# Kernel tuning notes

Measured on AMD Instinct MI355X. Metric: run time of the kernel, lower is better.

Reference implementation:

```python
import jax, jax.numpy as jnp
import numpy as np
from jax import lax

B, S, I, H = 64, 512, 1024, 1024


def _lstm_dir(x, W_ih, W_hh, b_ih, b_hh):
    # x: [B, S, I] -> hidden states [B, S, H]
    # Precompute input projections for all timesteps in one GEMM.
    xg = jnp.einsum('bsi,gi->bsg', x, W_ih) + b_ih + b_hh  # [B, S, 4H]
    Whh_T = W_hh.T  # [H, 4H]
    h0 = jnp.zeros((x.shape[0], W_hh.shape[1]), dtype=x.dtype)
    c0 = jnp.zeros_like(h0)

    def step(carry, xg_t):
        h, c = carry
        g = xg_t + h @ Whh_T  # [B, 4H]
        i_g, f_g, g_g, o_g = jnp.split(g, 4, axis=-1)  # PyTorch gate order i,f,g,o
        i_g = jax.nn.sigmoid(i_g)
        f_g = jax.nn.sigmoid(f_g)
        g_g = jnp.tanh(g_g)
        o_g = jax.nn.sigmoid(o_g)
        c = f_g * c + i_g * g_g
        h = o_g * jnp.tanh(c)
        return (h, c), h

    _, hs = lax.scan(step, (h0, c0), jnp.swapaxes(xg, 0, 1))  # hs: [S, B, H]
    return jnp.swapaxes(hs, 0, 1)


def setup_inputs() -> dict:
    key = jax.random.key(0)
    ks = jax.random.split(key, 10)
    s = 1.0 / np.sqrt(H)  # PyTorch LSTMCell init scale
    return {
        'forward_x': jax.random.normal(ks[0], (B, S, I), jnp.float32),
        'backward_x': jax.random.normal(ks[1], (B, S, I), jnp.float32),
        'W_ih_f': jax.random.uniform(ks[2], (4 * H, I), jnp.float32, -s, s),
        'W_hh_f': jax.random.uniform(ks[3], (4 * H, H), jnp.float32, -s, s),
        'b_ih_f': jax.random.uniform(ks[4], (4 * H,), jnp.float32, -s, s),
        'b_hh_f': jax.random.uniform(ks[5], (4 * H,), jnp.float32, -s, s),
        'W_ih_b': jax.random.uniform(ks[6], (4 * H, I), jnp.float32, -s, s),
        'W_hh_b': jax.random.uniform(ks[7], (4 * H, H), jnp.float32, -s, s),
        'b_ih_b': jax.random.uniform(ks[8], (4 * H,), jnp.float32, -s, s),
        'b_hh_b': jax.random.uniform(ks[9], (4 * H,), jnp.float32, -s, s),
    }


def reference(forward_x, backward_x, W_ih_f, W_hh_f, b_ih_f, b_hh_f,
              W_ih_b, W_hh_b, b_ih_b, b_hh_b):
    fwd = _lstm_dir(forward_x, W_ih_f, W_hh_f, b_ih_f, b_hh_f)
    # Backward direction consumes backward_x from the last timestep to the
    # first and writes hidden states back at their original positions,
    # i.e. run on the time-reversed sequence and reverse the outputs.
    bwd = _lstm_dir(backward_x[:, ::-1, :], W_ih_b, W_hh_b, b_ih_b, b_hh_b)[:, ::-1, :]
    return fwd, bwd
```

## Files before the change

kernel.cpp:

```cpp
#include <hip/hip_runtime.h>
#include <hip/hip_bf16.h>
#include <cstdint>


typedef __bf16 bf16_t;
typedef bf16_t bf16x8 __attribute__((ext_vector_type(8)));
typedef float  f32x4  __attribute__((ext_vector_type(4)));

#define DEVI __device__ __forceinline__

constexpr int Bb = 64, Ss = 512, Ii = 1024, Hh = 1024;
constexpr size_t WS_FLAGS  = 0;
constexpr size_t WS_HRING  = 4096;
constexpr size_t WS_XBF    = 1ull << 20;
constexpr size_t XBF_BYTES = 2ull * Ss * Bb * Ii * 2;
constexpr size_t WS_NEED_XBF = WS_XBF + XBF_BYTES;
constexpr int LDS_TOTAL = 163840;

DEVI float fast_sig(float x) {
  float z = __expf(-fabsf(x));
  float r = __builtin_amdgcn_rcpf(1.f + z);
  return x >= 0.f ? r : z * r;
}
DEVI float fast_tanh(float x) {
  float z = __expf(-2.f * fabsf(x));
  float r = (1.f - z) * __builtin_amdgcn_rcpf(1.f + z);
  return x >= 0.f ? r : -r;
}
DEVI bf16x8 cvt8(f32x4 a, f32x4 b) {
  bf16x8 r;
  r[0] = (bf16_t)a[0]; r[1] = (bf16_t)a[1]; r[2] = (bf16_t)a[2]; r[3] = (bf16_t)a[3];
  r[4] = (bf16_t)b[0]; r[5] = (bf16_t)b[1]; r[6] = (bf16_t)b[2]; r[7] = (bf16_t)b[3];
  return r;
}
DEVI f32x4 mfma16(bf16x8 a, bf16x8 b, f32x4 c) {
  return __builtin_amdgcn_mfma_f32_16x16x32_bf16(a, b, c, 0, 0, 0);
}

#define GLDS16(g, s)                                                           \
  __builtin_amdgcn_global_load_lds(                                            \
      (const __attribute__((address_space(1))) void*)(const void*)(g),         \
      (__attribute__((address_space(3))) void*)(void*)(s), 16, 0, 0)
#define GLDS16_COH(g, s)                                                       \
  __builtin_amdgcn_global_load_lds(                                            \
      (const __attribute__((address_space(1))) void*)(const void*)(g),         \
      (__attribute__((address_space(3))) void*)(void*)(s), 16, 0, 17)
#define WAIT_LGKM0 asm volatile("s_waitcnt lgkmcnt(0)" ::: "memory")
#define WAIT_VM(n) asm volatile("s_waitcnt vmcnt(" #n ")" ::: "memory")
#define BARRIER_RAW                                                            \
  do { __builtin_amdgcn_s_barrier(); __builtin_amdgcn_sched_barrier(0); } while (0)

__global__ void k_init(int* flags) {
  int i = threadIdx.x;
  if (i < 256) flags[i] = 0;
}

__global__ void k_convx(const float* __restrict__ xf, const float* __restrict__ xb,
                        bf16_t* __restrict__ dst) {
  size_t og = (size_t)blockIdx.x * blockDim.x + threadIdx.x;
  int i8  = (int)(og & 127);
  int b   = (int)((og >> 7) & 63);
  int t   = (int)((og >> 13) & 511);
  int dir = (int)(og >> 22);
  const float* src = (dir ? xb : xf) + (((size_t)b * Ss + t) * Ii + (size_t)i8 * 8);
  f32x4 a = *(const f32x4*)src;
  f32x4 c = *(const f32x4*)(src + 4);
  *(bf16x8*)(dst + og * 8) = cvt8(a, c);
}

template <bool XBF>
__global__ void __launch_bounds__(512, 2)
k_lstm(const float* __restrict__ xf, const float* __restrict__ xb,
       const float* __restrict__ Wih_f, const float* __restrict__ Whh_f,
       const float* __restrict__ bih_f, const float* __restrict__ bhh_f,
       const float* __restrict__ Wih_b, const float* __restrict__ Whh_b,
       const float* __restrict__ bih_b, const float* __restrict__ bhh_b,
       float* __restrict__ out,
       const bf16_t* __restrict__ xbfin, bf16_t* __restrict__ hring,
       int* __restrict__ flags) {
  extern __shared__ char lds[];
  char* PA = lds;
  char* PB = lds + 65536;
  float* part = (float*)(lds + 131072);

  const int tid = threadIdx.x;
  const int bid = blockIdx.x;
  const int dir = bid & 1;
  const int db  = bid >> 1;
  const int n0  = db * 8;
  const int w   = tid >> 6, l = tid & 63;
  const int u   = l >> 4, l15 = l & 15;
  const int m   = w & 1;
  const int kq  = w >> 1;

  const float* Wih = dir ? Wih_b : Wih_f;
  const float* Whh = dir ? Whh_b : Whh_f;
  const float* bih = dir ? bih_b : bih_f;
  const float* bhh = dir ? bhh_b : bhh_f;
  const float* x32 = dir ? xb : xf;
  const bf16_t* xbase = xbfin + (size_t)dir * Ss * Bb * Ii;
  bf16_t* hr = hring + (size_t)dir * 2 * Bb * Hh;
  float* outD = out + (size_t)dir * Bb * Ss * Hh;
  int* myflags = flags + dir * 128;

  bf16x8 wr[2][2][4][2];
#pragma unroll
  for (int mat = 0; mat < 2; ++mat)
#pragma unroll
    for (int p = 0; p < 2; ++p)
#pragma unroll
      for (int ks = 0; ks < 4; ++ks)
#pragma unroll
        for (int nt = 0; nt < 2; ++nt) {
          int c = nt * 16 + l15;
          int j = (c >> 3) * 1024 + n0 + (c & 7);
          int k = p * 512 + kq * 128 + ks * 32 + u * 8;
          const float* sp = (mat ? Whh : Wih) + (size_t)j * 1024 + k;
          wr[mat][p][ks][nt] = cvt8(*(const f32x4*)sp, *(const f32x4*)(sp + 4));
        }

  const int eb = tid >> 3, en = tid & 7;
  const int nj = n0 + en;
  float bi0 = bih[nj] + bhh[nj];
  float bi1 = bih[1024 + nj] + bhh[1024 + nj];
  float bi2 = bih[2048 + nj] + bhh[2048 + nj];
  float bi3 = bih[3072 + nj] + bhh[3072 + nj];

  int aoff0[4], aoff1[4];
#pragma unroll
  for (int ks = 0; ks < 4; ++ks) {
    int r0 = m * 32 + l15;
    int r1 = r0 + 16;
    int sl = kq * 16 + ks * 4 + u;
    aoff0[ks] = r0 * 1024 + ((sl ^ (r0 & 7)) << 4);
    aoff1[ks] = r1 * 1024 + ((sl ^ (r1 & 7)) << 4);
  }

  auto STAGE_DMA = [&](char* panel, const bf16_t* srcb) {
#pragma unroll
    for (int i = 0; i < 8; ++i) {
      const bf16_t* gp = srcb + (size_t)(w * 8 + i) * 1024 + ((l ^ i) << 3);
      char* sp = panel + (w * 8 + i) * 1024;
      GLDS16(gp, sp);
    }
  };
  auto STAGE_H = [&](char* panel, const bf16_t* srcb) {
#pragma unroll
    for (int i = 0; i < 8; ++i) {
      const bf16_t* gp = srcb + (size_t)(w * 8 + i) * 1024 + ((l ^ i) << 3);
      char* sp = panel + (w * 8 + i) * 1024;
      GLDS16_COH(gp, sp);
    }
  };
  auto STAGE_XF = [&](char* panel, const float* srcb) {
#pragma unroll
    for (int i = 0; i < 8; ++i) {
      int r = w * 8 + i;
      const float* sp = srcb + (size_t)r * (Ss * Ii) + ((l ^ i) << 3);
      f32x4 a = *(const f32x4*)sp;
      f32x4 b = *(const f32x4*)(sp + 4);
      *(bf16x8*)(panel + r * 1024 + l * 16) = cvt8(a, b);
    }
  };

  f32x4 acc00, acc01, acc10, acc11;
#define COMPUTE(panel, matC, pC)                                               \
  do {                                                                         \
    _Pragma("unroll") for (int ks = 0; ks < 4; ++ks) {                         \
      bf16x8 a0_ = *(const bf16x8*)((panel) + aoff0[ks]);                      \
      bf16x8 a1_ = *(const bf16x8*)((panel) + aoff1[ks]);                      \
      acc00 = mfma16(a0_, wr[matC][pC][ks][0], acc00);                         \
      acc01 = mfma16(a0_, wr[matC][pC][ks][1], acc01);                         \
      acc10 = mfma16(a1_, wr[matC][pC][ks][0], acc10);                         \
      acc11 = mfma16(a1_, wr[matC][pC][ks][1], acc11);                         \
    }                                                                          \
  } while (0)

  float c_reg = 0.f;

  {
    int t0 = dir ? (Ss - 1) : 0;
    if constexpr (XBF) STAGE_DMA(PA, xbase + (size_t)t0 * (Bb * Ii));
    else               STAGE_XF(PA, x32 + (size_t)t0 * Ii);
    WAIT_VM(0); WAIT_LGKM0; BARRIER_RAW;
  }

  for (int step = 0; step < Ss; ++step) {
    const int t  = dir ? (Ss - 1 - step) : step;
    const int tn = dir ? (Ss - 2 - step) : (step + 1);
    const bf16_t* hbase = hr + (size_t)((step - 1) & 1) * (Bb * Hh);

    acc00 = f32x4{0.f, 0.f, 0.f, 0.f}; acc01 = acc00; acc10 = acc00; acc11 = acc00;

    if constexpr (XBF) STAGE_DMA(PB, xbase + (size_t)t * (Bb * Ii) + 512);
    else               STAGE_XF(PB, x32 + (size_t)t * Ii + 512);
    COMPUTE(PA, 0, 0);
    WAIT_LGKM0;
    if (step > 0 && tid < 128) {
      const int* fp = &myflags[tid];
      while (__hip_atomic_load(fp, __ATOMIC_RELAXED, __HIP_MEMORY_SCOPE_AGENT) < step) {
      }
    }
    BARRIER_RAW;
    if (step > 0) {
      STAGE_H(PA, hbase);
      WAIT_VM(8);
      BARRIER_RAW;
    } else {
      WAIT_VM(0); BARRIER_RAW;
    }
    COMPUTE(PB, 0, 1);
    WAIT_LGKM0; BARRIER_RAW;
    if (step > 0) {
      STAGE_H(PB, hbase + 512);
      WAIT_VM(8); BARRIER_RAW;
      COMPUTE(PA, 1, 0);
      WAIT_LGKM0; BARRIER_RAW;
    }
    if (step < Ss - 1) {
      if constexpr (XBF) STAGE_DMA(PA, xbase + (size_t)tn * (Bb * Ii));
      else               STAGE_XF(PA, x32 + (size_t)tn * Ii);
    }
    if (step > 0) {
      if (step < Ss - 1) { WAIT_VM(8); } else { WAIT_VM(0); }
      BARRIER_RAW;
      COMPUTE(PB, 1, 1);
    }
    WAIT_LGKM0; BARRIER_RAW;

#pragma unroll
    for (int rr = 0; rr < 2; ++rr)
#pragma unroll
      for (int nt = 0; nt < 2; ++nt) {
        f32x4 a = (rr == 0) ? (nt == 0 ? acc00 : acc01) : (nt == 0 ? acc10 : acc11);
#pragma unroll
        for (int q = 0; q < 4; ++q) {
          int R = m * 32 + rr * 16 + u * 4 + q;
          int C = nt * 16 + l15;
          part[(kq * 64 + R) * 32 + (C ^ ((R & 7) << 2))] = a[q];
        }
      }
    WAIT_LGKM0; BARRIER_RAW;

    {
      const int sk = (eb & 7) << 2;
      float g0 = bi0, g1 = bi1, g2 = bi2, g3 = bi3;
#pragma unroll
      for (int q = 0; q < 4; ++q) {
        const float* pp = &part[(q * 64 + eb) * 32];
        g0 += pp[en ^ sk]; g1 += pp[(8 + en) ^ sk];
        g2 += pp[(16 + en) ^ sk]; g3 += pp[(24 + en) ^ sk];
      }
      float ig = fast_sig(g0), fg = fast_sig(g1);
      float gg = fast_tanh(g2), og = fast_sig(g3);
      c_reg = fg * c_reg + ig * gg;
      float h = og * fast_tanh(c_reg);
      outD[(size_t)eb * (Ss * Hh) + (size_t)t * Hh + n0 + en] = h;
      float hn = __shfl_xor(h, 1);
      if (!(tid & 1)) {
        union { bf16_t b[2]; uint32_t u32; } pk;
        pk.b[0] = (bf16_t)h; pk.b[1] = (bf16_t)hn;
        uint32_t* dst = (uint32_t*)&hr[(size_t)(step & 1) * (Bb * Hh) +
                                       (size_t)eb * Hh + n0 + en];
        __hip_atomic_store(dst, pk.u32, __ATOMIC_RELAXED, __HIP_MEMORY_SCOPE_AGENT);
      }
    }
    WAIT_VM(0); WAIT_LGKM0; BARRIER_RAW;
    if (tid == 0) {
      __hip_atomic_store(&myflags[db], step + 1, __ATOMIC_RELAXED,
                         __HIP_MEMORY_SCOPE_AGENT);
    }
  }
#undef COMPUTE
}

extern "C" void kernel_launch(void* const* d_in, const int* in_sizes, int n_in,
                              void* d_out, int out_size, void* d_ws, size_t ws_size,
                              hipStream_t stream) {
  (void)in_sizes; (void)n_in; (void)out_size;
  const float* xf    = (const float*)d_in[0];
  const float* xb    = (const float*)d_in[1];
  const float* Wih_f = (const float*)d_in[2];
  const float* Whh_f = (const float*)d_in[3];
  const float* bih_f = (const float*)d_in[4];
  const float* bhh_f = (const float*)d_in[5];
  const float* Wih_b = (const float*)d_in[6];
  const float* Whh_b = (const float*)d_in[7];
  const float* bih_b = (const float*)d_in[8];
  const float* bhh_b = (const float*)d_in[9];
  float* outp = (float*)d_out;
  char* ws = (char*)d_ws;
  int* flagsp = (int*)(ws + WS_FLAGS);
  bf16_t* hringp = (bf16_t*)(ws + WS_HRING);
  const bf16_t* xbfp = (const bf16_t*)(ws + WS_XBF);
  const bool use_xbf = ws_size >= WS_NEED_XBF;

  hipLaunchKernelGGL(k_init, dim3(1), dim3(256), 0, stream, flagsp);
  if (use_xbf) {
    hipLaunchKernelGGL(k_convx, dim3(32768), dim3(256), 0, stream,
                       xf, xb, (bf16_t*)(ws + WS_XBF));
  }

  void* args[] = {&xf, &xb, &Wih_f, &Whh_f, &bih_f, &bhh_f,
                  &Wih_b, &Whh_b, &bih_b, &bhh_b,
                  &outp, &xbfp, &hringp, &flagsp};
  if (use_xbf) {
    void (*kp)(const float*, const float*, const float*, const float*,
               const float*, const float*, const float*, const float*,
               const float*, const float*, float*, const bf16_t*, bf16_t*, int*) =
        k_lstm<true>;
    hipFuncSetAttribute((const void*)kp, hipFuncAttributeMaxDynamicSharedMemorySize,
                        LDS_TOTAL);
    hipLaunchCooperativeKernel((const void*)kp, dim3(256), dim3(512), args,
                               LDS_TOTAL, stream);
  } else {
    void (*kp)(const float*, const float*, const float*, const float*,
               const float*, const float*, const float*, const float*,
               const float*, const float*, float*, const bf16_t*, bf16_t*, int*) =
        k_lstm<false>;
    hipFuncSetAttribute((const void*)kp, hipFuncAttributeMaxDynamicSharedMemorySize,
                        LDS_TOTAL);
    hipLaunchCooperativeKernel((const void*)kp, dim3(256), dim3(512), args,
                               LDS_TOTAL, stream);
  }
}
```

Before: 3.439 ms.

## Prefetch both x panels for next step after publishing h, and widen h stores

Restructures the per-step schedule of the persistent LSTM kernel. After the step's hidden state is published and its flag set, both input-panel halves for the next timestep are staged into LDS, so the x-projection MFMAs at the start of a step run without waiting and the h loads are issued together with a single wait. Several barriers and partial vmcnt waits are removed. The h ring store is widened to 64-bit atomic stores via an extra shuffle, halving the number of store instructions. The x prefetch now sits on the recurrence critical path only after the flag is set, and the removed fine-grained overlap between h loads and compute may add latency.

```diff
diff --git a/kernel.cpp b/kernel.cpp
--- a/kernel.cpp
+++ b/kernel.cpp
@@ -32,6 +32,11 @@
   r[0] = (bf16_t)a[0]; r[1] = (bf16_t)a[1]; r[2] = (bf16_t)a[2]; r[3] = (bf16_t)a[3];
   r[4] = (bf16_t)b[0]; r[5] = (bf16_t)b[1]; r[6] = (bf16_t)b[2]; r[7] = (bf16_t)b[3];
   return r;
+}
+DEVI uint32_t pk_bf16(float lo, float hi) {
+  union { bf16_t b[2]; uint32_t u; } x;
+  x.b[0] = (bf16_t)lo; x.b[1] = (bf16_t)hi;
+  return x.u;
 }
 DEVI f32x4 mfma16(bf16x8 a, bf16x8 b, f32x4 c) {
   return __builtin_amdgcn_mfma_f32_16x16x32_bf16(a, b, c, 0, 0, 0);
@@ -46,7 +51,7 @@
       (const __attribute__((address_space(1))) void*)(const void*)(g),         \
       (__attribute__((address_space(3))) void*)(void*)(s), 16, 0, 17)
 #define WAIT_LGKM0 asm volatile("s_waitcnt lgkmcnt(0)" ::: "memory")
-#define WAIT_VM(n) asm volatile("s_waitcnt vmcnt(" #n ")" ::: "memory")
+#define WAIT_VM0   asm volatile("s_waitcnt vmcnt(0)" ::: "memory")
 #define BARRIER_RAW                                                            \
   do { __builtin_amdgcn_s_barrier(); __builtin_amdgcn_sched_barrier(0); } while (0)
 
@@ -180,9 +185,13 @@
 
   {
     int t0 = dir ? (Ss - 1) : 0;
-    if constexpr (XBF) STAGE_DMA(PA, xbase + (size_t)t0 * (Bb * Ii));
-    else               STAGE_XF(PA, x32 + (size_t)t0 * Ii);
-    WAIT_VM(0); WAIT_LGKM0; BARRIER_RAW;
+    if constexpr (XBF) {
+      STAGE_DMA(PA, xbase + (size_t)t0 * (Bb * Ii));
+      STAGE_DMA(PB, xbase + (size_t)t0 * (Bb * Ii) + 512);
+    } else {
+      STAGE_XF(PA, x32 + (size_t)t0 * Ii);
+      STAGE_XF(PB, x32 + (size_t)t0 * Ii + 512);
+    }
   }
 
   for (int step = 0; step < Ss; ++step) {
@@ -190,43 +199,29 @@
     const int tn = dir ? (Ss - 2 - step) : (step + 1);
     const bf16_t* hbase = hr + (size_t)((step - 1) & 1) * (Bb * Hh);
 
+    WAIT_VM0; WAIT_LGKM0; BARRIER_RAW;
+
     acc00 = f32x4{0.f, 0.f, 0.f, 0.f}; acc01 = acc00; acc10 = acc00; acc11 = acc00;
 
-    if constexpr (XBF) STAGE_DMA(PB, xbase + (size_t)t * (Bb * Ii) + 512);
-    else               STAGE_XF(PB, x32 + (size_t)t * Ii + 512);
     COMPUTE(PA, 0, 0);
+    COMPUTE(PB, 0, 1);
     WAIT_LGKM0;
+
     if (step > 0 && tid < 128) {
       const int* fp = &myflags[tid];
       while (__hip_atomic_load(fp, __ATOMIC_RELAXED, __HIP_MEMORY_SCOPE_AGENT) < step) {
       }
     }
     BARRIER_RAW;
+
     if (step > 0) {
       STAGE_H(PA, hbase);
-      WAIT_VM(8);
-      BARRIER_RAW;
-    } else {
-      WAIT_VM(0); BARRIER_RAW;
-    }
-    COMPUTE(PB, 0, 1);
-    WAIT_LGKM0; BARRIER_RAW;
-    if (step > 0) {
       STAGE_H(PB, hbase + 512);
-      WAIT_VM(8); BARRIER_RAW;
+      WAIT_VM0; BARRIER_RAW;
       COMPUTE(PA, 1, 0);
-      WAIT_LGKM0; BARRIER_RAW;
-    }
-    if (step < Ss - 1) {
-      if constexpr (XBF) STAGE_DMA(PA, xbase + (size_t)tn * (Bb * Ii));
-      else               STAGE_XF(PA, x32 + (size_t)tn * Ii);
-    }
-    if (step > 0) {
-      if (step < Ss - 1) { WAIT_VM(8); } else { WAIT_VM(0); }
-      BARRIER_RAW;
       COMPUTE(PB, 1, 1);
-    }
-    WAIT_LGKM0; BARRIER_RAW;
+      WAIT_LGKM0;
+    }
 
 #pragma unroll
     for (int rr = 0; rr < 2; ++rr)
@@ -256,19 +251,30 @@
       c_reg = fg * c_reg + ig * gg;
       float h = og * fast_tanh(c_reg);
       outD[(size_t)eb * (Ss * Hh) + (size_t)t * Hh + n0 + en] = h;
-      float hn = __shfl_xor(h, 1);
-      if (!(tid & 1)) {
-        union { bf16_t b[2]; uint32_t u32; } pk;
-        pk.b[0] = (bf16_t)h; pk.b[1] = (bf16_t)hn;
-        uint32_t* dst = (uint32_t*)&hr[(size_t)(step & 1) * (Bb * Hh) +
-                                       (size_t)eb * Hh + n0 + en];
-        __hip_atomic_store(dst, pk.u32, __ATOMIC_RELAXED, __HIP_MEMORY_SCOPE_AGENT);
-      }
-    }
-    WAIT_VM(0); WAIT_LGKM0; BARRIER_RAW;
+      uint32_t p01 = pk_bf16(h, __shfl_xor(h, 1));
+      uint32_t p23 = __shfl_xor(p01, 2);
+      if ((en & 3) == 0) {
+        uint64_t q8 = (uint64_t)p01 | ((uint64_t)p23 << 32);
+        uint64_t* dst = (uint64_t*)&hr[(size_t)(step & 1) * (Bb * Hh) +
+                                       (size_t)eb * Hh + n0 + (en & 4)];
+        __hip_atomic_store(dst, q8, __ATOMIC_RELAXED, __HIP_MEMORY_SCOPE_AGENT);
+      }
+    }
+
+    WAIT_VM0; BARRIER_RAW;
     if (tid == 0) {
       __hip_atomic_store(&myflags[db], step + 1, __ATOMIC_RELAXED,
                          __HIP_MEMORY_SCOPE_AGENT);
+    }
+
+    if (step < Ss - 1) {
+      if constexpr (XBF) {
+        STAGE_DMA(PA, xbase + (size_t)tn * (Bb * Ii));
+        STAGE_DMA(PB, xbase + (size_t)tn * (Bb * Ii) + 512);
+      } else {
+        STAGE_XF(PA, x32 + (size_t)tn * Ii);
+        STAGE_XF(PB, x32 + (size_t)tn * Ii + 512);
+      }
     }
   }
 #undef COMPUTE
```

New measurement: 3.510 ms. 2.1% more time.
